# Kernel tuning notes

Hardware: AMD Instinct MI355X
Metric: run time of the kernel (lower is better)

The kernel has to match this reference:

```python
import jax, jax.numpy as jnp
import numpy as np

B, S, C, H = 8, 1024, 512, 8
DH = C // H  # channels per head


def setup_inputs() -> dict:
    key = jax.random.key(0)
    ks = jax.random.split(key, 10)
    s = 1.0 / np.sqrt(C)
    return {
        "pe_lin_encoding": jax.random.normal(ks[0], (B, S, C), jnp.float32),
        "pe_lin_skip": jax.random.normal(ks[1], (B, S, C), jnp.float32),
        "Wq": jax.random.normal(ks[2], (C, C), jnp.float32) * s,
        "bq": jax.random.normal(ks[3], (C,), jnp.float32) * s,
        "Wk": jax.random.normal(ks[4], (C, C), jnp.float32) * s,
        "bk": jax.random.normal(ks[5], (C,), jnp.float32) * s,
        "Wv": jax.random.normal(ks[6], (C, C), jnp.float32) * s,
        "bv": jax.random.normal(ks[7], (C,), jnp.float32) * s,
        "Wo": jax.random.normal(ks[8], (C, C), jnp.float32) * s,
        "bo": jax.random.normal(ks[9], (C,), jnp.float32) * s,
    }


def reference(pe_lin_encoding, pe_lin_skip, Wq, bq, Wk, bk, Wv, bv, Wo, bo):
    # flatten trailing dims (already [B, S, C] here)
    x = pe_lin_encoding.reshape(pe_lin_encoding.shape[0], pe_lin_encoding.shape[1], -1)
    # torch Linear convention: y = x @ W^T + b, W is [out, in]
    q = jnp.einsum("bsc,oc->bso", x, Wq) + bq
    k = jnp.einsum("bsc,oc->bso", x, Wk) + bk
    v = jnp.einsum("bsc,oc->bso", x, Wv) + bv
    # split heads: [B, S, H, DH] -> attention per head
    q = q.reshape(B, S, H, DH)
    k = k.reshape(B, S, H, DH)
    v = v.reshape(B, S, H, DH)
    scale = 1.0 / np.sqrt(DH)
    scores = jnp.einsum("bqhd,bkhd->bhqk", q, k) * scale  # [B,H,S,S]
    attn = jax.nn.softmax(scores, axis=-1)
    ctx = jnp.einsum("bhqk,bkhd->bqhd", attn, v).reshape(B, S, C)
    out = jnp.einsum("bsc,oc->bso", ctx, Wo) + bo
    return out + pe_lin_skip
```

## Files before the change

kernel.cpp:

```cpp
#include <hip/hip_runtime.h>
#include <hip/hip_bf16.h>

typedef unsigned short u16;
typedef unsigned int u32;

constexpr int B  = 8;
constexpr int S  = 1024;
constexpr int C  = 512;
constexpr int H  = 8;
constexpr int DH = 64;
constexpr int M  = B * S;

typedef __attribute__((ext_vector_type(8))) short bf16x8;
typedef __attribute__((ext_vector_type(4))) float f32x4;
typedef __attribute__((ext_vector_type(16))) float f32x16;
typedef __attribute__((ext_vector_type(4))) u32 u32x4;

#define GLOBAL_AS __attribute__((address_space(1)))
#define LDS_AS    __attribute__((address_space(3)))

#define QSCALE 0.1803368867f

__device__ __forceinline__ float bf2f(u16 u) {
    return __uint_as_float(((u32)u) << 16);
}
__device__ __forceinline__ u16 f2bf(float f) {
    u32 u = __float_as_uint(f);
    u += 0x7fffu + ((u >> 16) & 1u);
    return (u16)(u >> 16);
}
__device__ __forceinline__ u32 pack2(float a, float b) {
    return (u32)f2bf(a) | ((u32)f2bf(b) << 16);
}
__device__ __forceinline__ u32 cvtpk(float a, float b) {
    u32 d;
    asm("v_cvt_pk_bf16_f32 %0, %1, %2" : "=v"(d) : "v"(a), "v"(b));
    return d;
}
__device__ __forceinline__ void async_cp16(const u16* g, u16* l) {
    __builtin_amdgcn_global_load_lds((const GLOBAL_AS void*)g, (LDS_AS void*)l, 16, 0, 0);
}
__device__ __forceinline__ f32x16 zero16() {
    f32x16 z;
    #pragma unroll
    for (int i = 0; i < 16; i++) z[i] = 0.f;
    return z;
}

constexpr int NX4 = M * C / 4;
constexpr int NW4 = C * C / 4;

__global__ __launch_bounds__(256) void cvt_kernel(
    const float* __restrict__ x,
    const float* __restrict__ wq, const float* __restrict__ wk,
    const float* __restrict__ wv, const float* __restrict__ wo,
    u16* __restrict__ xb, u16* __restrict__ wqkv, u16* __restrict__ wob)
{
    const int i = blockIdx.x * 256 + threadIdx.x;
    const float* src; u16* dst; int off;
    if      (i < NX4)          { src = x;  dst = xb;           off = i; }
    else if (i < NX4 +   NW4)  { src = wq; dst = wqkv;         off = i - NX4; }
    else if (i < NX4 + 2*NW4)  { src = wk; dst = wqkv + C*C;   off = i - NX4 -   NW4; }
    else if (i < NX4 + 3*NW4)  { src = wv; dst = wqkv + 2*C*C; off = i - NX4 - 2*NW4; }
    else                       { src = wo; dst = wob;          off = i - NX4 - 3*NW4; }
    float4 v = ((const float4*)src)[off];
    uint2 p; p.x = pack2(v.x, v.y); p.y = pack2(v.z, v.w);
    ((uint2*)dst)[off] = p;
}

__global__ __launch_bounds__(256) void qkv_gemm(
    const u16* __restrict__ xb, const u16* __restrict__ wqkv,
    const float* __restrict__ bq, const float* __restrict__ bk,
    const float* __restrict__ bv,
    u16* __restrict__ Qo, u16* __restrict__ Ko, u16* __restrict__ Vo)
{
    __shared__ alignas(16) u16 smem[128 * 136];
    u16* const Asm = smem;
    u16* const Bsm = smem + 128 * 64;

    const int mTile = blockIdx.x * 128;
    const int nTile = blockIdx.y * 128;
    const int t = threadIdx.x, lane = t & 63, w = t >> 6;
    const int ql = lane & 15, quad = lane >> 4;
    const int wm = (w & 1) * 64, wn = (w >> 1) * 64;

    f32x4 acc[4][4];
    #pragma unroll
    for (int i = 0; i < 4; i++)
        #pragma unroll
        for (int j = 0; j < 4; j++) acc[i][j] = (f32x4){0.f, 0.f, 0.f, 0.f};

    for (int k0 = 0; k0 < C; k0 += 64) {
        __syncthreads();
        #pragma unroll
        for (int q = 0; q < 4; q++) {
            const int chunk = q * 256 + t;
            const int row = chunk >> 3, c8 = (chunk & 7) * 8;
            async_cp16(xb   + (size_t)(mTile + row) * C + k0 + c8, &Asm[row * 64 + c8]);
            async_cp16(wqkv + (size_t)(nTile + row) * C + k0 + c8, &Bsm[row * 64 + c8]);
        }
        __syncthreads();

        #pragma unroll
        for (int ks = 0; ks < 64; ks += 32) {
            bf16x8 af[4], bfr[4];
            #pragma unroll
            for (int i = 0; i < 4; i++)
                af[i] = *(const bf16x8*)&Asm[(wm + i*16 + ql) * 64 + ks + quad*8];
            #pragma unroll
            for (int j = 0; j < 4; j++)
                bfr[j] = *(const bf16x8*)&Bsm[(wn + j*16 + ql) * 64 + ks + quad*8];
            #pragma unroll
            for (int i = 0; i < 4; i++)
                #pragma unroll
                for (int j = 0; j < 4; j++)
                    acc[i][j] = __builtin_amdgcn_mfma_f32_16x16x32_bf16(af[i], bfr[j], acc[i][j], 0, 0, 0);
        }
    }

    const int z = nTile >> 9;
    const int nBase = nTile & 511;
    if (z == 2) {
        __syncthreads();
        u16* const T = smem;
        #pragma unroll
        for (int j = 0; j < 4; j++) {
            const int n = wn + j*16 + ql;
            const float bj = bv[nBase + n];
            #pragma unroll
            for (int i = 0; i < 4; i++)
                #pragma unroll
                for (int r = 0; r < 4; r++)
                    T[n * 136 + wm + i*16 + quad*4 + r] = f2bf(acc[i][j][r] + bj);
        }
        __syncthreads();
        const int bb = mTile >> 10, ssBase = mTile & 1023;
        #pragma unroll
        for (int q = 0; q < 8; q++) {
            const int c = q * 256 + t;
            const int row = c >> 4, col = (c & 15) * 8;
            const int o = nBase + row, h = o >> 6, d = o & 63;
            *(float4*)(Vo + ((size_t)((bb*H + h) * DH + d)) * S + ssBase + col) =
                *(const float4*)&T[row * 136 + col];
        }
    } else {
        const float* bias = (z == 0) ? bq : bk;
        u16* dst          = (z == 0) ? Qo : Ko;
        const float sc    = (z == 0) ? QSCALE : 1.0f;
        #pragma unroll
        for (int j = 0; j < 4; j++) {
            const int o = nBase + wn + j*16 + ql;
            const float bj = bias[o];
            const int h = o >> 6, d = o & 63;
            #pragma unroll
            for (int i = 0; i < 4; i++) {
                #pragma unroll
                for (int r = 0; r < 4; r++) {
                    const int m = mTile + wm + i*16 + quad*4 + r;
                    const int bb = m >> 10, ss = m & 1023;
                    dst[(size_t)((bb*H + h) * S + ss) * DH + d] = f2bf((acc[i][j][r] + bj) * sc);
                }
            }
        }
    }
}

__global__ __launch_bounds__(256) void attn_kernel(
    const u16* __restrict__ Qo,
    const u16* __restrict__ Ko,
    const u16* __restrict__ Vo,
    u16* __restrict__ ctx)
{
    __shared__ alignas(16) u16 KV[2][2][64 * 64];

    const int g = blockIdx.x;
    const int xcd = g & 7, slot = g >> 3;
    const int bh = xcd * 8 + (slot >> 3);
    const int qt = slot & 7;

    const int t = threadIdx.x;
    const int lane = t & 63, w = t >> 6;
    const int l31 = lane & 31, hi = lane >> 5;
    const int sxh8 = ((l31 & 7) ^ hi) << 3;
    const int kRow = l31 * 64;

    const u16* __restrict__ Qb = Qo + (size_t)bh * S * DH;
    const u16* __restrict__ Kb = Ko + (size_t)bh * S * DH;
    const u16* __restrict__ Vt = Vo + (size_t)bh * DH * S;

    const int qrow = qt * 128 + w * 32 + l31;
    bf16x8 qf[4];
    #pragma unroll
    for (int ks = 0; ks < 4; ks++)
        qf[ks] = *(const bf16x8*)(Qb + (size_t)qrow * DH + ks * 16 + hi * 8);

    bf16x8 onesf;
    #pragma unroll
    for (int i = 0; i < 8; i++) onesf[i] = (short)0x3F80;

    f32x16 acc[2], accl;
    acc[0] = zero16(); acc[1] = zero16(); accl = zero16();

    float4 kreg[2], vreg[2];
    const int srow0 = t >> 3, scc = t & 7;
    const int scol = ((scc ^ (srow0 & 7)) << 3);

    auto LOADT = [&](int k0) {
        #pragma unroll
        for (int q2 = 0; q2 < 2; q2++) {
            const int row = q2 * 32 + srow0;
            kreg[q2] = *(const float4*)(Kb + (size_t)(k0 + row) * DH + scc * 8);
            vreg[q2] = *(const float4*)(Vt + (size_t)row * S + k0 + scc * 8);
        }
    };
    auto STORET = [&](int buf) {
        #pragma unroll
        for (int q2 = 0; q2 < 2; q2++) {
            const int row = q2 * 32 + srow0;
            *(float4*)&KV[buf][0][row * 64 + scol] = kreg[q2];
            *(float4*)&KV[buf][1][row * 64 + scol] = vreg[q2];
        }
    };

    LOADT(0);
    #pragma unroll 2
    for (int k0 = 0; k0 < S; k0 += 64) {
        const int buf = (k0 >> 6) & 1;
        STORET(buf);
        __syncthreads();
        if (k0 + 64 < S) LOADT(k0 + 64);
        const u16* Ks = KV[buf][0];
        const u16* Vs = KV[buf][1];

        #pragma unroll
        for (int kt = 0; kt < 2; kt++) {
            f32x16 sc = zero16();
            #pragma unroll
            for (int ks = 0; ks < 4; ks++) {
                const bf16x8 kf = *(const bf16x8*)&Ks[kRow + kt * 2048 + ((ks << 4) ^ sxh8)];
                sc = __builtin_amdgcn_mfma_f32_32x32x16_bf16(kf, qf[ks], sc, 0, 0, 0);
            }
            #pragma unroll
            for (int s = 0; s < 2; s++) {
                u32 x0 = cvtpk(exp2f(sc[8*s+0]), exp2f(sc[8*s+1]));
                u32 x1 = cvtpk(exp2f(sc[8*s+2]), exp2f(sc[8*s+3]));
                u32 y0 = cvtpk(exp2f(sc[8*s+4]), exp2f(sc[8*s+5]));
                u32 y1 = cvtpk(exp2f(sc[8*s+6]), exp2f(sc[8*s+7]));
                asm("v_permlane32_swap_b32 %0, %1" : "+v"(x0), "+v"(y0));
                asm("v_permlane32_swap_b32 %0, %1" : "+v"(x1), "+v"(y1));
                u32x4 pw; pw.x = x0; pw.y = x1; pw.z = y0; pw.w = y1;
                const bf16x8 pa = __builtin_bit_cast(bf16x8, pw);

                const int ccol = (((kt * 4 + s * 2) << 3) ^ sxh8);
                #pragma unroll
                for (int nt = 0; nt < 2; nt++) {
                    const bf16x8 vf = *(const bf16x8*)&Vs[kRow + nt * 2048 + ccol];
                    acc[nt] = __builtin_amdgcn_mfma_f32_32x32x16_bf16(pa, vf, acc[nt], 0, 0, 0);
                }
                accl = __builtin_amdgcn_mfma_f32_32x32x16_bf16(pa, onesf, accl, 0, 0, 0);
            }
        }
    }

    const int b_ = bh >> 3, h = bh & 7;
    const int qbase2 = qt * 128 + w * 32 + 4 * hi;
    #pragma unroll
    for (int r = 0; r < 16; r++) {
        const float inv = 1.0f / accl[r];
        const int srow = qbase2 + (r & 3) + 8 * (r >> 2);
        const size_t base = ((size_t)(b_ * S + srow)) * C + h * DH + l31;
        ctx[base]      = f2bf(acc[0][r] * inv);
        ctx[base + 32] = f2bf(acc[1][r] * inv);
    }
}

__global__ __launch_bounds__(256) void out_gemm(
    const u16* __restrict__ ctx, const u16* __restrict__ wob,
    const float* __restrict__ bo, const float* __restrict__ skip,
    float* __restrict__ out)
{
    __shared__ alignas(16) u16 Asm[128 * 64];
    __shared__ alignas(16) u16 Bsm[128 * 64];

    const int mTile = blockIdx.x * 128;
    const int nTile = blockIdx.y * 128;
    const int t = threadIdx.x, lane = t & 63, w = t >> 6;
    const int ql = lane & 15, quad = lane >> 4;
    const int wm = (w & 1) * 64, wn = (w >> 1) * 64;

    f32x4 acc[4][4];
    #pragma unroll
    for (int i = 0; i < 4; i++)
        #pragma unroll
        for (int j = 0; j < 4; j++) acc[i][j] = (f32x4){0.f, 0.f, 0.f, 0.f};

    for (int k0 = 0; k0 < C; k0 += 64) {
        __syncthreads();
        #pragma unroll
        for (int q = 0; q < 4; q++) {
            const int chunk = q * 256 + t;
            const int row = chunk >> 3, c8 = (chunk & 7) * 8;
            async_cp16(ctx + (size_t)(mTile + row) * C + k0 + c8, &Asm[row * 64 + c8]);
            async_cp16(wob + (size_t)(nTile + row) * C + k0 + c8, &Bsm[row * 64 + c8]);
        }
        __syncthreads();

        #pragma unroll
        for (int ks = 0; ks < 64; ks += 32) {
            bf16x8 af[4], bfr[4];
            #pragma unroll
            for (int i = 0; i < 4; i++)
                af[i] = *(const bf16x8*)&Asm[(wm + i*16 + ql) * 64 + ks + quad*8];
            #pragma unroll
            for (int j = 0; j < 4; j++)
                bfr[j] = *(const bf16x8*)&Bsm[(wn + j*16 + ql) * 64 + ks + quad*8];
            #pragma unroll
            for (int i = 0; i < 4; i++)
                #pragma unroll
                for (int j = 0; j < 4; j++)
                    acc[i][j] = __builtin_amdgcn_mfma_f32_16x16x32_bf16(af[i], bfr[j], acc[i][j], 0, 0, 0);
        }
    }

    #pragma unroll
    for (int j = 0; j < 4; j++) {
        const int o = nTile + wn + j*16 + ql;
        const float bj = bo[o];
        #pragma unroll
        for (int i = 0; i < 4; i++) {
            #pragma unroll
            for (int r = 0; r < 4; r++) {
                const int m = mTile + wm + i*16 + quad*4 + r;
                const size_t idx = (size_t)m * C + o;
                out[idx] = acc[i][j][r] + bj + skip[idx];
            }
        }
    }
}

extern "C" void kernel_launch(void* const* d_in, const int* in_sizes, int n_in,
                              void* d_out, int out_size, void* d_ws, size_t ws_size,
                              hipStream_t stream) {
    (void)in_sizes; (void)n_in; (void)out_size; (void)ws_size;
    const float* x    = (const float*)d_in[0];
    const float* skip = (const float*)d_in[1];
    const float* Wq   = (const float*)d_in[2];
    const float* bq   = (const float*)d_in[3];
    const float* Wk   = (const float*)d_in[4];
    const float* bk   = (const float*)d_in[5];
    const float* Wv   = (const float*)d_in[6];
    const float* bv   = (const float*)d_in[7];
    const float* Wo   = (const float*)d_in[8];
    const float* bo   = (const float*)d_in[9];
    float* out = (float*)d_out;

    u16* xb   = (u16*)d_ws;
    u16* wqkv = xb   + (size_t)M * C;
    u16* wob  = wqkv + (size_t)3 * C * C;
    u16* Qo   = wob  + (size_t)C * C;
    u16* Ko   = Qo   + (size_t)B * H * S * DH;
    u16* Vo   = Ko   + (size_t)B * H * S * DH;
    u16* ctx  = xb;

    cvt_kernel<<<dim3((NX4 + 4 * NW4) / 256), 256, 0, stream>>>(
        x, Wq, Wk, Wv, Wo, xb, wqkv, wob);
    qkv_gemm<<<dim3(M / 128, 1536 / 128), 256, 0, stream>>>(
        xb, wqkv, bq, bk, bv, Qo, Ko, Vo);
    attn_kernel<<<dim3(512), 256, 0, stream>>>(Qo, Ko, Vo, ctx);
    out_gemm<<<dim3(M / 128, C / 128), 256, 0, stream>>>(
        ctx, wob, bo, skip, out);
}
```

Measured before the change: 196.9 us.

## Split attention keys across wave pairs with async LDS loads and VALU row sums

The attention kernel now gives each block 64 queries instead of 128 and doubles the grid to 1024 blocks. Inside a block, wave pairs each process half of the key range into their own LDS buffers, and the partial accumulators are merged through LDS at the end. K/V tiles are fetched with async global-to-LDS copies instead of a register-staged double buffer. The softmax denominator is summed on the VALU with a cross-half shuffle, replacing the extra MFMA against a ones vector. The goal is more parallelism and fewer MFMAs, at the cost of losing the load/compute overlap of the old prefetch and adding an extra reduction step.

```diff
diff --git a/kernel.cpp b/kernel.cpp
--- a/kernel.cpp
+++ b/kernel.cpp
@@ -175,11 +175,12 @@
 
     const int g = blockIdx.x;
     const int xcd = g & 7, slot = g >> 3;
-    const int bh = xcd * 8 + (slot >> 3);
-    const int qt = slot & 7;
+    const int bh = xcd * 8 + (slot >> 4);
+    const int qt = slot & 15;
 
     const int t = threadIdx.x;
     const int lane = t & 63, w = t >> 6;
+    const int qg = w & 1, kg = w >> 1;
     const int l31 = lane & 31, hi = lane >> 5;
     const int sxh8 = ((l31 & 7) ^ hi) << 3;
     const int kRow = l31 * 64;
@@ -188,89 +189,96 @@
     const u16* __restrict__ Kb = Ko + (size_t)bh * S * DH;
     const u16* __restrict__ Vt = Vo + (size_t)bh * DH * S;
 
-    const int qrow = qt * 128 + w * 32 + l31;
+    const int qrow = qt * 64 + qg * 32 + l31;
     bf16x8 qf[4];
     #pragma unroll
     for (int ks = 0; ks < 4; ks++)
         qf[ks] = *(const bf16x8*)(Qb + (size_t)qrow * DH + ks * 16 + hi * 8);
 
-    bf16x8 onesf;
-    #pragma unroll
-    for (int i = 0; i < 8; i++) onesf[i] = (short)0x3F80;
-
-    f32x16 acc[2], accl;
-    acc[0] = zero16(); acc[1] = zero16(); accl = zero16();
-
-    float4 kreg[2], vreg[2];
-    const int srow0 = t >> 3, scc = t & 7;
-    const int scol = ((scc ^ (srow0 & 7)) << 3);
-
-    auto LOADT = [&](int k0) {
-        #pragma unroll
-        for (int q2 = 0; q2 < 2; q2++) {
-            const int row = q2 * 32 + srow0;
-            kreg[q2] = *(const float4*)(Kb + (size_t)(k0 + row) * DH + scc * 8);
-            vreg[q2] = *(const float4*)(Vt + (size_t)row * S + k0 + scc * 8);
-        }
-    };
-    auto STORET = [&](int buf) {
-        #pragma unroll
-        for (int q2 = 0; q2 < 2; q2++) {
-            const int row = q2 * 32 + srow0;
-            *(float4*)&KV[buf][0][row * 64 + scol] = kreg[q2];
-            *(float4*)&KV[buf][1][row * 64 + scol] = vreg[q2];
-        }
-    };
-
-    LOADT(0);
-    #pragma unroll 2
-    for (int k0 = 0; k0 < S; k0 += 64) {
-        const int buf = (k0 >> 6) & 1;
-        STORET(buf);
-        __syncthreads();
-        if (k0 + 64 < S) LOADT(k0 + 64);
-        const u16* Ks = KV[buf][0];
-        const u16* Vs = KV[buf][1];
-
-        #pragma unroll
-        for (int kt = 0; kt < 2; kt++) {
+    f32x16 acc[2];
+    acc[0] = zero16(); acc[1] = zero16();
+    float dsum = 0.f;
+
+    u16* const Kh = KV[kg][0];
+    u16* const Vh = KV[kg][1];
+    const int tp = t & 127;
+    const int kBase = kg * 512;
+
+    for (int it = 0; it < 8; ++it) {
+        const int k0 = kBase + it * 64;
+        if (it) __syncthreads();
+        #pragma unroll
+        for (int q = 0; q < 4; ++q) {
+            const int gi = q * 128 + tp;
+            const int row = gi >> 3, cc = gi & 7;
+            const int c = cc ^ (row & 7);
+            async_cp16(Kb + (size_t)(k0 + row) * DH + c * 8, &Kh[gi * 8]);
+            async_cp16(Vt + (size_t)row * S + k0 + c * 8,    &Vh[gi * 8]);
+        }
+        __syncthreads();
+
+        #pragma unroll
+        for (int kt = 0; kt < 2; ++kt) {
             f32x16 sc = zero16();
             #pragma unroll
-            for (int ks = 0; ks < 4; ks++) {
-                const bf16x8 kf = *(const bf16x8*)&Ks[kRow + kt * 2048 + ((ks << 4) ^ sxh8)];
+            for (int ks = 0; ks < 4; ++ks) {
+                const bf16x8 kf = *(const bf16x8*)&Kh[kRow + kt * 2048 + ((ks << 4) ^ sxh8)];
                 sc = __builtin_amdgcn_mfma_f32_32x32x16_bf16(kf, qf[ks], sc, 0, 0, 0);
             }
             #pragma unroll
-            for (int s = 0; s < 2; s++) {
-                u32 x0 = cvtpk(exp2f(sc[8*s+0]), exp2f(sc[8*s+1]));
-                u32 x1 = cvtpk(exp2f(sc[8*s+2]), exp2f(sc[8*s+3]));
-                u32 y0 = cvtpk(exp2f(sc[8*s+4]), exp2f(sc[8*s+5]));
-                u32 y1 = cvtpk(exp2f(sc[8*s+6]), exp2f(sc[8*s+7]));
+            for (int s = 0; s < 2; ++s) {
+                float e0 = exp2f(sc[8*s+0]), e1 = exp2f(sc[8*s+1]);
+                float e2 = exp2f(sc[8*s+2]), e3 = exp2f(sc[8*s+3]);
+                float e4 = exp2f(sc[8*s+4]), e5 = exp2f(sc[8*s+5]);
+                float e6 = exp2f(sc[8*s+6]), e7 = exp2f(sc[8*s+7]);
+                dsum += ((e0 + e1) + (e2 + e3)) + ((e4 + e5) + (e6 + e7));
+                u32 x0 = cvtpk(e0, e1), x1 = cvtpk(e2, e3);
+                u32 y0 = cvtpk(e4, e5), y1 = cvtpk(e6, e7);
                 asm("v_permlane32_swap_b32 %0, %1" : "+v"(x0), "+v"(y0));
                 asm("v_permlane32_swap_b32 %0, %1" : "+v"(x1), "+v"(y1));
                 u32x4 pw; pw.x = x0; pw.y = x1; pw.z = y0; pw.w = y1;
                 const bf16x8 pa = __builtin_bit_cast(bf16x8, pw);
 
                 const int ccol = (((kt * 4 + s * 2) << 3) ^ sxh8);
-                #pragma unroll
-                for (int nt = 0; nt < 2; nt++) {
-                    const bf16x8 vf = *(const bf16x8*)&Vs[kRow + nt * 2048 + ccol];
-                    acc[nt] = __builtin_amdgcn_mfma_f32_32x32x16_bf16(pa, vf, acc[nt], 0, 0, 0);
-                }
-                accl = __builtin_amdgcn_mfma_f32_32x32x16_bf16(pa, onesf, accl, 0, 0, 0);
+                acc[0] = __builtin_amdgcn_mfma_f32_32x32x16_bf16(
+                    pa, *(const bf16x8*)&Vh[kRow + ccol], acc[0], 0, 0, 0);
+                acc[1] = __builtin_amdgcn_mfma_f32_32x32x16_bf16(
+                    pa, *(const bf16x8*)&Vh[kRow + 2048 + ccol], acc[1], 0, 0, 0);
             }
         }
     }
 
-    const int b_ = bh >> 3, h = bh & 7;
-    const int qbase2 = qt * 128 + w * 32 + 4 * hi;
-    #pragma unroll
-    for (int r = 0; r < 16; r++) {
-        const float inv = 1.0f / accl[r];
-        const int srow = qbase2 + (r & 3) + 8 * (r >> 2);
-        const size_t base = ((size_t)(b_ * S + srow)) * C + h * DH + l31;
-        ctx[base]      = f2bf(acc[0][r] * inv);
-        ctx[base + 32] = f2bf(acc[1][r] * inv);
+    float dtot = dsum + __shfl_xor(dsum, 32);
+
+    __syncthreads();
+    float* F = (float*)&KV[0][0][0];
+    if (kg == 1) {
+        #pragma unroll
+        for (int r = 0; r < 16; ++r) F[r * 128 + qg * 64 + lane] = acc[0][r];
+        #pragma unroll
+        for (int r = 0; r < 16; ++r) F[(16 + r) * 128 + qg * 64 + lane] = acc[1][r];
+        F[32 * 128 + qg * 64 + lane] = dtot;
+    }
+    __syncthreads();
+    if (kg == 0) {
+        #pragma unroll
+        for (int r = 0; r < 16; ++r) acc[0][r] += F[r * 128 + qg * 64 + lane];
+        #pragma unroll
+        for (int r = 0; r < 16; ++r) acc[1][r] += F[(16 + r) * 128 + qg * 64 + lane];
+        dtot += F[32 * 128 + qg * 64 + lane];
+
+        const int b_ = bh >> 3, h = bh & 7;
+        const int qbase2 = qt * 64 + qg * 32 + 4 * hi;
+        #pragma unroll
+        for (int r = 0; r < 16; ++r) {
+            const int cr = (r & 3) + 8 * (r >> 2);
+            const float dr = __shfl(dtot, 4 * hi + cr);
+            const float inv = 1.0f / dr;
+            const int srow = qbase2 + cr;
+            const size_t base = ((size_t)(b_ * S + srow)) * C + h * DH + l31;
+            ctx[base]      = f2bf(acc[0][r] * inv);
+            ctx[base + 32] = f2bf(acc[1][r] * inv);
+        }
     }
 }
 
@@ -366,7 +374,7 @@
         x, Wq, Wk, Wv, Wo, xb, wqkv, wob);
     qkv_gemm<<<dim3(M / 128, 1536 / 128), 256, 0, stream>>>(
         xb, wqkv, bq, bk, bv, Qo, Ko, Vo);
-    attn_kernel<<<dim3(512), 256, 0, stream>>>(Qo, Ko, Vo, ctx);
+    attn_kernel<<<dim3(1024), 256, 0, stream>>>(Qo, Ko, Vo, ctx);
     out_gemm<<<dim3(M / 128, C / 128), 256, 0, stream>>>(
         ctx, wob, bo, skip, out);
 }
```

After: 174.6 us. -11.3%, faster.
